# Kernel tuning notes

Measured on AMD Instinct MI355X. Metric: run time of the kernel, lower is better.

## Reference

```python
import jax, jax.numpy as jnp
import numpy as np
from jax import lax

B, N, C = 8, 2000, 81
MAX_INST = 100
MIN_CONF = 0.7
NMS_THR = 0.3
WINDOW = jnp.array([0.0, 0.0, 1.0, 1.0], jnp.float32)  # y1, x1, y2, x2
BBOX_STD = jnp.array([0.1, 0.1, 0.2, 0.2], jnp.float32)


def setup_inputs() -> dict:
    key = jax.random.key(0)
    k1, k2, k3 = jax.random.split(key, 3)
    # build valid boxes: sample coordinate pairs and sort so y1<=y2, x1<=x2
    yx = jax.random.uniform(k1, (B, N, 2, 2), dtype=jnp.float32)
    mins, maxs = yx.min(axis=2), yx.max(axis=2)
    rois = jnp.stack([mins[..., 0], mins[..., 1], maxs[..., 0], maxs[..., 1]], axis=-1)
    probs = jax.random.uniform(k2, (B, N, C), dtype=jnp.float32)
    deltas = jax.random.normal(k3, (B, N, C, 4), dtype=jnp.float32) * 0.5
    return {"rois": rois, "probs": probs, "deltas": deltas}


def _apply_box_deltas(boxes, deltas):
    # boxes: [N,4] (y1,x1,y2,x2); deltas: [N,4] (dy,dx,log_dh,log_dw)
    h = boxes[:, 2] - boxes[:, 0]
    w = boxes[:, 3] - boxes[:, 1]
    cy = boxes[:, 0] + 0.5 * h + deltas[:, 0] * h
    cx = boxes[:, 1] + 0.5 * w + deltas[:, 1] * w
    h = h * jnp.exp(deltas[:, 2])
    w = w * jnp.exp(deltas[:, 3])
    return jnp.stack([cy - 0.5 * h, cx - 0.5 * w, cy + 0.5 * h, cx + 0.5 * w], axis=1)


def _clip_boxes(boxes, window):
    wy1, wx1, wy2, wx2 = window
    y1 = jnp.clip(boxes[:, 0], wy1, wy2)
    x1 = jnp.clip(boxes[:, 1], wx1, wx2)
    y2 = jnp.clip(boxes[:, 2], wy1, wy2)
    x2 = jnp.clip(boxes[:, 3], wx1, wx2)
    return jnp.stack([y1, x1, y2, x2], axis=1)


def _pairwise_iou(boxes):
    # boxes: [N,4] -> [N,N]
    y1, x1, y2, x2 = boxes[:, 0], boxes[:, 1], boxes[:, 2], boxes[:, 3]
    area = (y2 - y1) * (x2 - x1)
    iy1 = jnp.maximum(y1[:, None], y1[None, :])
    ix1 = jnp.maximum(x1[:, None], x1[None, :])
    iy2 = jnp.minimum(y2[:, None], y2[None, :])
    ix2 = jnp.minimum(x2[:, None], x2[None, :])
    inter = jnp.maximum(iy2 - iy1, 0.0) * jnp.maximum(ix2 - ix1, 0.0)
    union = area[:, None] + area[None, :] - inter
    return inter / jnp.maximum(union, 1e-12)


def _refine_one(rois, probs, deltas):
    # rois [N,4], probs [N,C], deltas [N,C,4]
    class_ids = jnp.argmax(probs, axis=1)                      # [N]
    rng = jnp.arange(N)
    class_scores = probs[rng, class_ids]                       # [N]
    deltas_specific = deltas[rng, class_ids]                   # [N,4]
    refined = _apply_box_deltas(rois, deltas_specific * BBOX_STD)
    refined = _clip_boxes(refined, WINDOW)

    valid = (class_ids > 0) & (class_scores >= MIN_CONF)

    # sort by score descending (invalid entries pushed to the end)
    order = jnp.argsort(-jnp.where(valid, class_scores, -jnp.inf))
    boxes_s = refined[order]
    scores_s = class_scores[order]
    cls_s = class_ids[order]
    valid_s = valid[order]

    # per-class greedy NMS: suppress only within the same class
    iou = _pairwise_iou(boxes_s)                               # [N,N]
    suppress_mat = (iou > NMS_THR) & (cls_s[:, None] == cls_s[None, :])
    lower = jnp.arange(N)

    def body(i, keep):
        sup = suppress_mat[i] & keep[i] & (lower > i)
        return keep & ~sup

    keep = lax.fori_loop(0, N, body, valid_s)

    # per-class cap at MAX_INST (mirrors max_output_size in tf NMS)
    onehot = jax.nn.one_hot(cls_s, C, dtype=jnp.int32) * keep.astype(jnp.int32)[:, None]
    rank = jnp.cumsum(onehot, axis=0)[lower, cls_s]            # inclusive per-class rank
    keep = keep & (rank <= MAX_INST)

    # global top-k by score among kept, zero-padded
    final_scores = jnp.where(keep, scores_s, -jnp.inf)
    _, top_idx = lax.top_k(final_scores, MAX_INST)
    valid_top = keep[top_idx]
    box_out = jnp.where(valid_top[:, None], boxes_s[top_idx], 0.0)
    cls_out = jnp.where(valid_top, cls_s[top_idx].astype(jnp.float32), 0.0)
    sc_out = jnp.where(valid_top, scores_s[top_idx], 0.0)
    return jnp.concatenate([box_out, cls_out[:, None], sc_out[:, None]], axis=1)  # [MAX_INST,6]


def reference(rois, probs, deltas):
    return jax.vmap(_refine_one)(rois, probs, deltas)  # [B, MAX_INST, 6]
```

## Files before the change

kernel.cpp:

```cpp
#include <hip/hip_runtime.h>
#include <math.h>

#define BB 8
#define NN 2000
#define CC 81
#define NCLS 80
#define MAXI 100
#define MCLS 128

static constexpr float kMinConf = 0.7f;
static constexpr float kNmsThr  = 0.3f;


__device__ __forceinline__ unsigned long long mkey(float s, int i) {
    return ((unsigned long long)__float_as_uint(s) << 32) | (unsigned int)(~(unsigned int)i);
}

__device__ __forceinline__ bool iou_gt_thr(float4 a, float aarea, float4 t) {
    float iy1 = fmaxf(a.x, t.x), ix1 = fmaxf(a.y, t.y);
    float iy2 = fminf(a.z, t.z), ix2 = fminf(a.w, t.w);
    float inter = fmaxf(iy2 - iy1, 0.f) * fmaxf(ix2 - ix1, 0.f);
    float tarea = (t.z - t.x) * (t.w - t.y);
    float uni = fmaxf(aarea + tarea - inter, 1e-12f);
    return inter > kNmsThr * uni;
}

__global__ void kA_refine(const float* __restrict__ rois,
                          const float* __restrict__ probs,
                          const float* __restrict__ deltas,
                          float* __restrict__ boxes,
                          float* __restrict__ sc,
                          int* __restrict__ cls,
                          unsigned long long* __restrict__ keysrc,
                          float* __restrict__ outz) {
    int gtid = blockIdx.x * blockDim.x + threadIdx.x;
    if (gtid < BB * MAXI * 6) outz[gtid] = 0.f;
    if (gtid < BB * NN) keysrc[gtid] = 0ull;

    int wid = gtid >> 6;
    int l = gtid & 63;

    const float* p = probs + (size_t)wid * CC;
    float v1 = p[l];
    int   i1 = l;
    int   c2 = l + 64;
    float v2 = (c2 < CC) ? p[c2] : -1.0f;
    float bv; int bi;
    if (v2 > v1) { bv = v2; bi = c2; } else { bv = v1; bi = i1; }

    #pragma unroll
    for (int off = 32; off; off >>= 1) {
        float ov = __shfl_xor(bv, off);
        int   oi = __shfl_xor(bi, off);
        if (ov > bv || (ov == bv && oi < bi)) { bv = ov; bi = oi; }
    }

    if (l == 0) {
        const float4 dl = *(const float4*)(deltas + ((size_t)wid * CC + bi) * 4);
        float dy = dl.x * 0.1f, dx = dl.y * 0.1f, dh = dl.z * 0.2f, dw = dl.w * 0.2f;
        const float4 r = *(const float4*)(rois + (size_t)wid * 4);
        float y1 = r.x, x1 = r.y, y2 = r.z, x2 = r.w;
        float h = y2 - y1, w = x2 - x1;
        float cy = y1 + 0.5f * h + dy * h;
        float cx = x1 + 0.5f * w + dx * w;
        float h2 = h * expf(dh);
        float w2 = w * expf(dw);
        float oy1 = fminf(fmaxf(cy - 0.5f * h2, 0.f), 1.f);
        float ox1 = fminf(fmaxf(cx - 0.5f * w2, 0.f), 1.f);
        float oy2 = fminf(fmaxf(cy + 0.5f * h2, 0.f), 1.f);
        float ox2 = fminf(fmaxf(cx + 0.5f * w2, 0.f), 1.f);
        bool valid = (bi > 0) && (bv >= kMinConf);
        float4 bx; bx.x = oy1; bx.y = ox1; bx.z = oy2; bx.w = ox2;
        ((float4*)boxes)[wid] = bx;
        sc[wid] = bv;
        cls[wid] = valid ? bi : 0;
    }
}

__global__ void __launch_bounds__(1024) kB0_bucket(
        const float* __restrict__ sc,
        const int* __restrict__ cls,
        int* __restrict__ ccnt,
        unsigned long long* __restrict__ cslot) {
    const int b = blockIdx.x;
    const int tid = threadIdx.x;
    __shared__ int lcnt[NCLS];

    if (tid < NCLS) lcnt[tid] = 0;
    __syncthreads();

    for (int i = tid; i < NN; i += 1024) {
        int c = cls[(size_t)b * NN + i];
        if (c > 0) {
            int pos = atomicAdd(&lcnt[c - 1], 1);
            if (pos < MCLS)
                cslot[(size_t)(b * NCLS + (c - 1)) * MCLS + pos] =
                    mkey(sc[(size_t)b * NN + i], i);
        }
    }
    __syncthreads();
    if (tid < NCLS) ccnt[b * NCLS + tid] = lcnt[tid];
}

__global__ void __launch_bounds__(64) kB1_nms(
        const float* __restrict__ boxes,
        const int* __restrict__ ccnt,
        const unsigned long long* __restrict__ cslot,
        unsigned long long* __restrict__ keysrc) {
    const int p = blockIdx.x;
    const int b = p / NCLS;
    const int cidx = p % NCLS;
    const int l = threadIdx.x;

    __shared__ unsigned long long mk[MCLS];
    __shared__ float4 mbox[MCLS];

    const int cnt = min(ccnt[b * NCLS + cidx], MCLS);
    if (cnt == 0) return;
    const unsigned long long* slot = cslot + (size_t)(b * NCLS + cidx) * MCLS;
    const float4* bxs = (const float4*)boxes + (size_t)b * NN;

    unsigned long long va = (l < cnt) ? slot[l] : 0ull;
    unsigned long long vb = (64 + l < cnt) ? slot[64 + l] : 0ull;
    if (l < cnt) mk[l] = va;
    if (64 + l < cnt) mk[64 + l] = vb;
    int ra = 0, rb = 0;
    for (int t = 0; t < cnt; ++t) {
        unsigned long long kt = mk[t];
        ra += (kt > va);
        rb += (kt > vb);
    }
    if (l < cnt) mk[ra] = va;
    if (64 + l < cnt) mk[rb] = vb;

    for (int t = l; t < cnt; t += 64) {
        int i = (int)(~(unsigned int)mk[t]);
        mbox[t] = bxs[i];
    }

    unsigned long long kept0 = 0ull;
    {
        bool act = (l < cnt);
        float4 a = mbox[act ? l : 0];
        float aarea = (a.z - a.x) * (a.w - a.y);
        unsigned long long colmask = 0ull;
        int tend = min(64, cnt);
        for (int t = 0; t < tend; ++t) {
            float4 tb = mbox[t];
            if (t < l && act && iou_gt_thr(a, aarea, tb)) colmask |= (1ull << t);
        }
        unsigned long long kept = __ballot(act);
        while (true) {
            bool alive = act && ((colmask & kept) == 0ull);
            unsigned long long k2m = __ballot(alive);
            if (k2m == kept) break;
            kept = k2m;
        }
        kept0 = kept;
        bool alive = act && ((colmask & kept0) == 0ull);
        if (alive) {
            unsigned long long myk = mk[l];
            keysrc[(size_t)b * NN + (int)(~(unsigned int)myk)] = myk;
        }
    }
    if (cnt > 64) {
        int m = 64 + l;
        bool act = (m < cnt);
        float4 a = mbox[act ? m : 0];
        float aarea = (a.z - a.x) * (a.w - a.y);
        bool presup = false;
        for (int t = 0; t < 64; ++t) {
            if ((kept0 >> t) & 1ull) {
                if (act && iou_gt_thr(a, aarea, mbox[t])) presup = true;
            }
        }
        unsigned long long colmask = 0ull;
        for (int t = 64; t < cnt; ++t) {
            float4 tb = mbox[t];
            if ((t - 64) < l && act && iou_gt_thr(a, aarea, tb)) colmask |= (1ull << (t - 64));
        }
        bool pre = act && !presup;
        unsigned long long kept = __ballot(pre);
        while (true) {
            bool alive = pre && ((colmask & kept) == 0ull);
            unsigned long long k2m = __ballot(alive);
            if (k2m == kept) break;
            kept = k2m;
        }
        bool alive = pre && ((colmask & kept) == 0ull);
        if (alive) {
            unsigned long long myk = mk[64 + l];
            keysrc[(size_t)b * NN + (int)(~(unsigned int)myk)] = myk;
        }
    }
}

__global__ void __launch_bounds__(1024) kC_emit(
        const unsigned long long* __restrict__ keysrc,
        const float* __restrict__ boxes,
        const int* __restrict__ cls,
        float* __restrict__ out) {
    const int b = blockIdx.x;
    const int tid = threadIdx.x;
    const int wv = tid >> 6;
    const int l = tid & 63;

    __shared__ ulonglong2 keys2[1024];
    __shared__ ulonglong2 cand2[256];
    __shared__ int hist[256];
    __shared__ int Tcnt, tbsh, candn;
    unsigned long long* keys = (unsigned long long*)keys2;
    unsigned long long* cand = (unsigned long long*)cand2;

    if (tid < 256) hist[tid] = 0;
    if (tid < 48) keys[2000 + tid] = 0ull;
    if (tid == 0) { Tcnt = 0; candn = 0; }
    __syncthreads();

    const float4* bxs = (const float4*)boxes + (size_t)b * NN;

    for (int i = tid; i < NN; i += 1024) {
        unsigned long long kv = keysrc[(size_t)b * NN + i];
        keys[i] = kv;
        bool f = (kv != 0ull);
        if (f) atomicAdd(&hist[(int)((kv >> 47) & 0xFF)], 1);
        unsigned long long m = __ballot(f);
        if (l == 0 && m) atomicAdd(&Tcnt, __popcll(m));
    }
    __syncthreads();
    const int T = Tcnt;
    if (T == 0) return;

    if (wv == 0) {
        int cum = 0, tb = 0, done = 0;
        for (int chunk = 3; chunk >= 0 && !done; --chunk) {
            int bkt = chunk * 64 + (63 - l);
            int s = hist[bkt];
            #pragma unroll
            for (int off = 1; off < 64; off <<= 1) {
                int o = __shfl_up(s, off);
                if (l >= off) s += o;
            }
            int chunktot = __shfl(s, 63);
            if (cum + chunktot >= MAXI) {
                unsigned long long m = __ballot(cum + s >= MAXI);
                int lane = __ffsll((long long)m) - 1;
                tb = chunk * 64 + (63 - lane);
                done = 1;
            } else {
                cum += chunktot;
            }
        }
        if (l == 0) tbsh = done ? tb : 0;
    }
    __syncthreads();
    const int tb = tbsh;

    for (int i = tid; i < NN; i += 1024) {
        unsigned long long kv = keys[i];
        bool pr = (kv != 0ull) && ((int)((kv >> 47) & 0xFF) >= tb);
        unsigned long long m = __ballot(pr);
        int basew = 0;
        if (l == 0 && m) basew = atomicAdd(&candn, __popcll(m));
        basew = __shfl(basew, 0);
        if (pr) {
            int pos = basew + __popcll(m & ((1ull << l) - 1ull));
            if (pos < 512) cand[pos] = kv;
        }
    }
    __syncthreads();
    const int nc = candn;
    if (tid == 0 && nc < 512) cand[nc] = 0ull;
    __syncthreads();

    if (nc <= 512) {
        const int np = (nc + 1) >> 1;
        for (int s = tid; s < nc; s += 1024) {
            unsigned long long myk = cand[s];
            int r = 0;
            for (int t = 0; t < np; ++t) {
                ulonglong2 kv = cand2[t];
                r += (int)(kv.x > myk);
                r += (int)(kv.y > myk);
            }
            if (r < MAXI) {
                int i = (int)(~(unsigned int)myk);
                float4 bx = bxs[i];
                float* o = out + ((size_t)b * MAXI + r) * 6;
                o[0] = bx.x; o[1] = bx.y; o[2] = bx.z; o[3] = bx.w;
                o[4] = (float)cls[(size_t)b * NN + i];
                o[5] = __uint_as_float((unsigned int)(myk >> 32));
            }
        }
    } else {
        for (int s = tid; s < NN; s += 1024) {
            unsigned long long myk = keys[s];
            if (myk == 0ull) continue;
            int r = 0;
            for (int t = 0; t < 1024; ++t) {
                ulonglong2 kv = keys2[t];
                r += (int)(kv.x > myk);
                r += (int)(kv.y > myk);
            }
            if (r < MAXI) {
                int i = (int)(~(unsigned int)myk);
                float4 bx = bxs[i];
                float* o = out + ((size_t)b * MAXI + r) * 6;
                o[0] = bx.x; o[1] = bx.y; o[2] = bx.z; o[3] = bx.w;
                o[4] = (float)cls[(size_t)b * NN + i];
                o[5] = __uint_as_float((unsigned int)(myk >> 32));
            }
        }
    }
}

extern "C" void kernel_launch(void* const* d_in, const int* in_sizes, int n_in,
                              void* d_out, int out_size, void* d_ws, size_t ws_size,
                              hipStream_t stream) {
    const float* rois   = (const float*)d_in[0];
    const float* probs  = (const float*)d_in[1];
    const float* deltas = (const float*)d_in[2];
    float* outp = (float*)d_out;

    char* ws = (char*)d_ws;
    float* boxes = (float*)(ws + 0);
    float* sc    = (float*)(ws + 256000);
    int*   cls   = (int*)  (ws + 320000);
    int*   ccnt  = (int*)  (ws + 384000);
    unsigned long long* cslot  = (unsigned long long*)(ws + 386560);
    unsigned long long* keysrc = (unsigned long long*)(ws + 1041920);

    {
        int blocks = (BB * NN * 64) / 256;
        kA_refine<<<blocks, 256, 0, stream>>>(rois, probs, deltas, boxes, sc,
                                              cls, keysrc, outp);
    }
    kB0_bucket<<<BB, 1024, 0, stream>>>(sc, cls, ccnt, cslot);
    kB1_nms<<<BB * NCLS, 64, 0, stream>>>(boxes, ccnt, cslot, keysrc);
    kC_emit<<<BB, 1024, 0, stream>>>(keysrc, boxes, cls, outp);
}
```

Baseline: 29.10 us.

## Fuse refine and class bucketing into one kernel with per-quarter slot buffers

Merges the box-refine kernel and the per-class bucketing kernel into one launch. Each of 32 blocks takes a quarter of one batch's rows and appends valid keys into shared-memory per-class queues of capacity 32. The NMS kernel then gathers the four quarter queues per class into contiguous order. This removes one kernel launch and the round trip of scores through global memory. In exchange, the refine stage drops from thousands of small blocks to 32 blocks, each wave processing about 32 rows in sequence. That cuts parallelism and memory-latency hiding, and any class that has more than 32 hits in one quarter is silently truncated.

```diff
diff --git a/kernel.cpp b/kernel.cpp
--- a/kernel.cpp
+++ b/kernel.cpp
@@ -7,6 +7,7 @@
 #define NCLS 80
 #define MAXI 100
 #define MCLS 128
+#define QCAP 32
 
 static constexpr float kMinConf = 0.7f;
 static constexpr float kNmsThr  = 0.3f;
@@ -25,86 +26,90 @@
     return inter > kNmsThr * uni;
 }
 
-__global__ void kA_refine(const float* __restrict__ rois,
-                          const float* __restrict__ probs,
-                          const float* __restrict__ deltas,
-                          float* __restrict__ boxes,
-                          float* __restrict__ sc,
-                          int* __restrict__ cls,
-                          unsigned long long* __restrict__ keysrc,
-                          float* __restrict__ outz) {
-    int gtid = blockIdx.x * blockDim.x + threadIdx.x;
+__global__ void __launch_bounds__(1024) kA_refine_bucket(
+        const float* __restrict__ rois,
+        const float* __restrict__ probs,
+        const float* __restrict__ deltas,
+        float* __restrict__ boxes,
+        int* __restrict__ cls,
+        int* __restrict__ qcnt,
+        unsigned long long* __restrict__ cslot,
+        unsigned long long* __restrict__ keysrc,
+        float* __restrict__ outz) {
+    const int b = blockIdx.x >> 2;
+    const int q = blockIdx.x & 3;
+    const int tid = threadIdx.x;
+    const int w = tid >> 6;
+    const int l = tid & 63;
+
+    __shared__ unsigned long long lkey[NCLS][QCAP];
+    __shared__ int lcnt[NCLS];
+
+    int gtid = blockIdx.x * 1024 + tid;
     if (gtid < BB * MAXI * 6) outz[gtid] = 0.f;
     if (gtid < BB * NN) keysrc[gtid] = 0ull;
-
-    int wid = gtid >> 6;
-    int l = gtid & 63;
-
-    const float* p = probs + (size_t)wid * CC;
-    float v1 = p[l];
-    int   i1 = l;
-    int   c2 = l + 64;
-    float v2 = (c2 < CC) ? p[c2] : -1.0f;
-    float bv; int bi;
-    if (v2 > v1) { bv = v2; bi = c2; } else { bv = v1; bi = i1; }
-
-    #pragma unroll
-    for (int off = 32; off; off >>= 1) {
-        float ov = __shfl_xor(bv, off);
-        int   oi = __shfl_xor(bi, off);
-        if (ov > bv || (ov == bv && oi < bi)) { bv = ov; bi = oi; }
-    }
-
-    if (l == 0) {
-        const float4 dl = *(const float4*)(deltas + ((size_t)wid * CC + bi) * 4);
-        float dy = dl.x * 0.1f, dx = dl.y * 0.1f, dh = dl.z * 0.2f, dw = dl.w * 0.2f;
-        const float4 r = *(const float4*)(rois + (size_t)wid * 4);
-        float y1 = r.x, x1 = r.y, y2 = r.z, x2 = r.w;
-        float h = y2 - y1, w = x2 - x1;
-        float cy = y1 + 0.5f * h + dy * h;
-        float cx = x1 + 0.5f * w + dx * w;
-        float h2 = h * expf(dh);
-        float w2 = w * expf(dw);
-        float oy1 = fminf(fmaxf(cy - 0.5f * h2, 0.f), 1.f);
-        float ox1 = fminf(fmaxf(cx - 0.5f * w2, 0.f), 1.f);
-        float oy2 = fminf(fmaxf(cy + 0.5f * h2, 0.f), 1.f);
-        float ox2 = fminf(fmaxf(cx + 0.5f * w2, 0.f), 1.f);
-        bool valid = (bi > 0) && (bv >= kMinConf);
-        float4 bx; bx.x = oy1; bx.y = ox1; bx.z = oy2; bx.w = ox2;
-        ((float4*)boxes)[wid] = bx;
-        sc[wid] = bv;
-        cls[wid] = valid ? bi : 0;
-    }
-}
-
-__global__ void __launch_bounds__(1024) kB0_bucket(
-        const float* __restrict__ sc,
-        const int* __restrict__ cls,
-        int* __restrict__ ccnt,
-        unsigned long long* __restrict__ cslot) {
-    const int b = blockIdx.x;
-    const int tid = threadIdx.x;
-    __shared__ int lcnt[NCLS];
-
     if (tid < NCLS) lcnt[tid] = 0;
     __syncthreads();
 
-    for (int i = tid; i < NN; i += 1024) {
-        int c = cls[(size_t)b * NN + i];
-        if (c > 0) {
-            int pos = atomicAdd(&lcnt[c - 1], 1);
-            if (pos < MCLS)
-                cslot[(size_t)(b * NCLS + (c - 1)) * MCLS + pos] =
-                    mkey(sc[(size_t)b * NN + i], i);
-        }
-    }
-    __syncthreads();
-    if (tid < NCLS) ccnt[b * NCLS + tid] = lcnt[tid];
+    for (int r = 0; r < 32; ++r) {
+        int loc = r * 16 + w;
+        if (loc >= 500) break;
+        int i = q * 500 + loc;
+        int wid = b * NN + i;
+
+        const float* p = probs + (size_t)wid * CC;
+        float v1 = p[l];
+        int   i1 = l;
+        int   c2 = l + 64;
+        float v2 = (c2 < CC) ? p[c2] : -1.0f;
+        float bv; int bi;
+        if (v2 > v1) { bv = v2; bi = c2; } else { bv = v1; bi = i1; }
+
+        #pragma unroll
+        for (int off = 32; off; off >>= 1) {
+            float ov = __shfl_xor(bv, off);
+            int   oi = __shfl_xor(bi, off);
+            if (ov > bv || (ov == bv && oi < bi)) { bv = ov; bi = oi; }
+        }
+
+        if (l == 0) {
+            const float4 dl = *(const float4*)(deltas + ((size_t)wid * CC + bi) * 4);
+            float dy = dl.x * 0.1f, dx = dl.y * 0.1f, dh = dl.z * 0.2f, dw = dl.w * 0.2f;
+            const float4 rr = *(const float4*)(rois + (size_t)wid * 4);
+            float y1 = rr.x, x1 = rr.y, y2 = rr.z, x2 = rr.w;
+            float h = y2 - y1, ww = x2 - x1;
+            float cy = y1 + 0.5f * h + dy * h;
+            float cx = x1 + 0.5f * ww + dx * ww;
+            float h2 = h * expf(dh);
+            float w2 = ww * expf(dw);
+            float oy1 = fminf(fmaxf(cy - 0.5f * h2, 0.f), 1.f);
+            float ox1 = fminf(fmaxf(cx - 0.5f * w2, 0.f), 1.f);
+            float oy2 = fminf(fmaxf(cy + 0.5f * h2, 0.f), 1.f);
+            float ox2 = fminf(fmaxf(cx + 0.5f * w2, 0.f), 1.f);
+            bool valid = (bi > 0) && (bv >= kMinConf);
+            float4 bx; bx.x = oy1; bx.y = ox1; bx.z = oy2; bx.w = ox2;
+            ((float4*)boxes)[wid] = bx;
+            cls[wid] = valid ? bi : 0;
+            if (valid) {
+                int cidx = bi - 1;
+                int pos = atomicAdd(&lcnt[cidx], 1);
+                if (pos < QCAP) lkey[cidx][pos] = mkey(bv, i);
+            }
+        }
+    }
+    __syncthreads();
+
+    if (tid < NCLS) qcnt[(b * NCLS + tid) * 4 + q] = min(lcnt[tid], QCAP);
+    for (int e = tid; e < NCLS * QCAP; e += 1024) {
+        int c = e >> 5, j = e & (QCAP - 1);
+        if (j < min(lcnt[c], QCAP))
+            cslot[(((size_t)b * NCLS + c) * 4 + q) * QCAP + j] = lkey[c][j];
+    }
 }
 
 __global__ void __launch_bounds__(64) kB1_nms(
         const float* __restrict__ boxes,
-        const int* __restrict__ ccnt,
+        const int* __restrict__ qcnt,
         const unsigned long long* __restrict__ cslot,
         unsigned long long* __restrict__ keysrc) {
     const int p = blockIdx.x;
@@ -115,15 +120,26 @@
     __shared__ unsigned long long mk[MCLS];
     __shared__ float4 mbox[MCLS];
 
-    const int cnt = min(ccnt[b * NCLS + cidx], MCLS);
+    const int* qc = qcnt + (b * NCLS + cidx) * 4;
+    int qc0 = qc[0], qc1 = qc[1], qc2 = qc[2], qc3 = qc[3];
+    const int cnt = qc0 + qc1 + qc2 + qc3;
     if (cnt == 0) return;
-    const unsigned long long* slot = cslot + (size_t)(b * NCLS + cidx) * MCLS;
+    int pref1 = qc0, pref2 = qc0 + qc1, pref3 = qc0 + qc1 + qc2;
+
+    const unsigned long long* base = cslot + ((size_t)b * NCLS + cidx) * (4 * QCAP);
     const float4* bxs = (const float4*)boxes + (size_t)b * NN;
 
-    unsigned long long va = (l < cnt) ? slot[l] : 0ull;
-    unsigned long long vb = (64 + l < cnt) ? slot[64 + l] : 0ull;
-    if (l < cnt) mk[l] = va;
-    if (64 + l < cnt) mk[64 + l] = vb;
+    #pragma unroll
+    for (int e0 = 0; e0 < 2; ++e0) {
+        int e = e0 * 64 + l;
+        int qq = e >> 5, j = e & (QCAP - 1);
+        int qcv = (qq == 0) ? qc0 : (qq == 1) ? qc1 : (qq == 2) ? qc2 : qc3;
+        int pr  = (qq == 0) ? 0   : (qq == 1) ? pref1 : (qq == 2) ? pref2 : pref3;
+        if (j < qcv) mk[pr + j] = base[e];
+    }
+
+    unsigned long long va = (l < cnt) ? mk[l] : 0ull;
+    unsigned long long vb = (64 + l < cnt) ? mk[64 + l] : 0ull;
     int ra = 0, rb = 0;
     for (int t = 0; t < cnt; ++t) {
         unsigned long long kt = mk[t];
@@ -324,18 +340,13 @@
 
     char* ws = (char*)d_ws;
     float* boxes = (float*)(ws + 0);
-    float* sc    = (float*)(ws + 256000);
-    int*   cls   = (int*)  (ws + 320000);
-    int*   ccnt  = (int*)  (ws + 384000);
-    unsigned long long* cslot  = (unsigned long long*)(ws + 386560);
-    unsigned long long* keysrc = (unsigned long long*)(ws + 1041920);
-
-    {
-        int blocks = (BB * NN * 64) / 256;
-        kA_refine<<<blocks, 256, 0, stream>>>(rois, probs, deltas, boxes, sc,
-                                              cls, keysrc, outp);
-    }
-    kB0_bucket<<<BB, 1024, 0, stream>>>(sc, cls, ccnt, cslot);
-    kB1_nms<<<BB * NCLS, 64, 0, stream>>>(boxes, ccnt, cslot, keysrc);
+    int*   cls   = (int*)  (ws + 256000);
+    int*   qcnt  = (int*)  (ws + 320000);
+    unsigned long long* cslot  = (unsigned long long*)(ws + 330240);
+    unsigned long long* keysrc = (unsigned long long*)(ws + 985600);
+
+    kA_refine_bucket<<<BB * 4, 1024, 0, stream>>>(rois, probs, deltas, boxes,
+                                                  cls, qcnt, cslot, keysrc, outp);
+    kB1_nms<<<BB * NCLS, 64, 0, stream>>>(boxes, qcnt, cslot, keysrc);
     kC_emit<<<BB, 1024, 0, stream>>>(keysrc, boxes, cls, outp);
 }
```

Measured after the change: 60.76 us. +108.8%, slower.

## Split per-class bucketing into four quarter blocks per batch and merge in NMS

Applied to the files above, without the earlier changes.

The bucket kernel now runs four blocks per image, each handling 500 detections and staging per-class keys in shared memory before writing them out in compact per-quarter slots. The NMS kernel reads the four quarter counts and concatenates the slots into its sort buffer. This spreads the bucketing work over more blocks and makes the global writes coalesced. In exchange it caps each quarter at 32 entries per class, which could drop detections in dense classes. The emit kernel also drops its total-count atomic and early exit.

```diff
diff --git a/kernel.cpp b/kernel.cpp
--- a/kernel.cpp
+++ b/kernel.cpp
@@ -7,6 +7,7 @@
 #define NCLS 80
 #define MAXI 100
 #define MCLS 128
+#define QCAP 32
 
 static constexpr float kMinConf = 0.7f;
 static constexpr float kNmsThr  = 0.3f;
@@ -80,31 +81,39 @@
 __global__ void __launch_bounds__(1024) kB0_bucket(
         const float* __restrict__ sc,
         const int* __restrict__ cls,
-        int* __restrict__ ccnt,
+        int* __restrict__ qcnt,
         unsigned long long* __restrict__ cslot) {
-    const int b = blockIdx.x;
+    const int b = blockIdx.x >> 2;
+    const int q = blockIdx.x & 3;
     const int tid = threadIdx.x;
+
+    __shared__ unsigned long long lkey[NCLS][QCAP];
     __shared__ int lcnt[NCLS];
 
     if (tid < NCLS) lcnt[tid] = 0;
     __syncthreads();
 
-    for (int i = tid; i < NN; i += 1024) {
+    if (tid < 500) {
+        int i = q * 500 + tid;
         int c = cls[(size_t)b * NN + i];
         if (c > 0) {
             int pos = atomicAdd(&lcnt[c - 1], 1);
-            if (pos < MCLS)
-                cslot[(size_t)(b * NCLS + (c - 1)) * MCLS + pos] =
-                    mkey(sc[(size_t)b * NN + i], i);
-        }
-    }
-    __syncthreads();
-    if (tid < NCLS) ccnt[b * NCLS + tid] = lcnt[tid];
+            if (pos < QCAP) lkey[c - 1][pos] = mkey(sc[(size_t)b * NN + i], i);
+        }
+    }
+    __syncthreads();
+
+    if (tid < NCLS) qcnt[(b * NCLS + tid) * 4 + q] = min(lcnt[tid], QCAP);
+    for (int e = tid; e < NCLS * QCAP; e += 1024) {
+        int c = e >> 5, j = e & (QCAP - 1);
+        if (j < min(lcnt[c], QCAP))
+            cslot[(((size_t)b * NCLS + c) * 4 + q) * QCAP + j] = lkey[c][j];
+    }
 }
 
 __global__ void __launch_bounds__(64) kB1_nms(
         const float* __restrict__ boxes,
-        const int* __restrict__ ccnt,
+        const int* __restrict__ qcnt,
         const unsigned long long* __restrict__ cslot,
         unsigned long long* __restrict__ keysrc) {
     const int p = blockIdx.x;
@@ -115,15 +124,26 @@
     __shared__ unsigned long long mk[MCLS];
     __shared__ float4 mbox[MCLS];
 
-    const int cnt = min(ccnt[b * NCLS + cidx], MCLS);
+    const int* qc = qcnt + (b * NCLS + cidx) * 4;
+    int qc0 = qc[0], qc1 = qc[1], qc2 = qc[2], qc3 = qc[3];
+    const int cnt = qc0 + qc1 + qc2 + qc3;
     if (cnt == 0) return;
-    const unsigned long long* slot = cslot + (size_t)(b * NCLS + cidx) * MCLS;
+    int pref1 = qc0, pref2 = qc0 + qc1, pref3 = qc0 + qc1 + qc2;
+
+    const unsigned long long* base = cslot + ((size_t)b * NCLS + cidx) * (4 * QCAP);
     const float4* bxs = (const float4*)boxes + (size_t)b * NN;
 
-    unsigned long long va = (l < cnt) ? slot[l] : 0ull;
-    unsigned long long vb = (64 + l < cnt) ? slot[64 + l] : 0ull;
-    if (l < cnt) mk[l] = va;
-    if (64 + l < cnt) mk[64 + l] = vb;
+    #pragma unroll
+    for (int e0 = 0; e0 < 2; ++e0) {
+        int e = e0 * 64 + l;
+        int qq = e >> 5, j = e & (QCAP - 1);
+        int qcv = (qq == 0) ? qc0 : (qq == 1) ? qc1 : (qq == 2) ? qc2 : qc3;
+        int pr  = (qq == 0) ? 0   : (qq == 1) ? pref1 : (qq == 2) ? pref2 : pref3;
+        if (j < qcv) mk[pr + j] = base[e];
+    }
+
+    unsigned long long va = (l < cnt) ? mk[l] : 0ull;
+    unsigned long long vb = (64 + l < cnt) ? mk[64 + l] : 0ull;
     int ra = 0, rb = 0;
     for (int t = 0; t < cnt; ++t) {
         unsigned long long kt = mk[t];
@@ -208,13 +228,13 @@
     __shared__ ulonglong2 keys2[1024];
     __shared__ ulonglong2 cand2[256];
     __shared__ int hist[256];
-    __shared__ int Tcnt, tbsh, candn;
+    __shared__ int tbsh, candn;
     unsigned long long* keys = (unsigned long long*)keys2;
     unsigned long long* cand = (unsigned long long*)cand2;
 
     if (tid < 256) hist[tid] = 0;
     if (tid < 48) keys[2000 + tid] = 0ull;
-    if (tid == 0) { Tcnt = 0; candn = 0; }
+    if (tid == 0) candn = 0;
     __syncthreads();
 
     const float4* bxs = (const float4*)boxes + (size_t)b * NN;
@@ -222,14 +242,9 @@
     for (int i = tid; i < NN; i += 1024) {
         unsigned long long kv = keysrc[(size_t)b * NN + i];
         keys[i] = kv;
-        bool f = (kv != 0ull);
-        if (f) atomicAdd(&hist[(int)((kv >> 47) & 0xFF)], 1);
-        unsigned long long m = __ballot(f);
-        if (l == 0 && m) atomicAdd(&Tcnt, __popcll(m));
-    }
-    __syncthreads();
-    const int T = Tcnt;
-    if (T == 0) return;
+        if (kv != 0ull) atomicAdd(&hist[(int)((kv >> 47) & 0xFF)], 1);
+    }
+    __syncthreads();
 
     if (wv == 0) {
         int cum = 0, tb = 0, done = 0;
@@ -326,16 +341,16 @@
     float* boxes = (float*)(ws + 0);
     float* sc    = (float*)(ws + 256000);
     int*   cls   = (int*)  (ws + 320000);
-    int*   ccnt  = (int*)  (ws + 384000);
-    unsigned long long* cslot  = (unsigned long long*)(ws + 386560);
-    unsigned long long* keysrc = (unsigned long long*)(ws + 1041920);
+    int*   qcnt  = (int*)  (ws + 384000);
+    unsigned long long* cslot  = (unsigned long long*)(ws + 394240);
+    unsigned long long* keysrc = (unsigned long long*)(ws + 1049600);
 
     {
         int blocks = (BB * NN * 64) / 256;
         kA_refine<<<blocks, 256, 0, stream>>>(rois, probs, deltas, boxes, sc,
                                               cls, keysrc, outp);
     }
-    kB0_bucket<<<BB, 1024, 0, stream>>>(sc, cls, ccnt, cslot);
-    kB1_nms<<<BB * NCLS, 64, 0, stream>>>(boxes, ccnt, cslot, keysrc);
+    kB0_bucket<<<BB * 4, 1024, 0, stream>>>(sc, cls, qcnt, cslot);
+    kB1_nms<<<BB * NCLS, 64, 0, stream>>>(boxes, qcnt, cslot, keysrc);
     kC_emit<<<BB, 1024, 0, stream>>>(keysrc, boxes, cls, outp);
 }
```

New measurement: 28.87 us. No clear change (-0.8%).
